# Optimization experiments

Hardware: AMD Instinct MI355X
Metric: run time of the kernel (lower is better)

## Reference

```python
import jax, jax.numpy as jnp
import numpy as np

V, E, H, Z = 32000, 512, 1024, 256
B, S, T = 64, 256, 64
BOS_ID, EOS_ID = 1, 2


def gru_cell(x_gates, h, W_hh, b_hh):
    # torch GRU gate order: r, z, n. x_gates: (B,3H) precomputed W_ih@x+b_ih.
    hg = h @ W_hh.T + b_hh
    xr, xz, xn = jnp.split(x_gates, 3, axis=-1)
    hr, hz, hn = jnp.split(hg, 3, axis=-1)
    r = jax.nn.sigmoid(xr + hr)
    z = jax.nn.sigmoid(xz + hz)
    n = jnp.tanh(xn + r * hn)
    return (1.0 - z) * n + z * h


def setup_inputs() -> dict:
    key = jax.random.key(0)
    ks = jax.random.split(key, 24)
    u = lambda k, sh: jax.random.uniform(k, sh, jnp.float32, -0.1, 0.1)
    n = lambda k, sh: jax.random.normal(k, sh, jnp.float32) * 0.05
    inp = {
        'input': jax.random.randint(ks[0], (S, B), 0, V),
        'eps': jax.random.normal(ks[1], (B, Z), jnp.float32),
        'emb_enc': u(ks[2], (V, E)).at[0].set(0.0),  # padding_idx=0
        'Wih_e': n(ks[3], (3 * H, E)), 'Whh_e': n(ks[4], (3 * H, H)),
        'bih_e': n(ks[5], (3 * H,)), 'bhh_e': n(ks[6], (3 * H,)),
        'W_enc': n(ks[7], (Z, H)), 'b_enc': n(ks[8], (Z,)),
        'W_loc': n(ks[9], (Z, Z)), 'b_loc': n(ks[10], (Z,)),
        'W_scale': n(ks[11], (Z, Z)), 'b_scale': n(ks[12], (Z,)),
        'emb_dec': u(ks[13], (V, E)).at[0].set(0.0),
        'W_dec': n(ks[14], (H, Z)), 'b_dec': n(ks[15], (H,)),
        'Wih_d': n(ks[16], (3 * H, E)), 'Whh_d': n(ks[17], (3 * H, H)),
        'bih_d': n(ks[18], (3 * H,)), 'bhh_d': n(ks[19], (3 * H,)),
        'W_voc': n(ks[20], (V, H)), 'b_voc': n(ks[21], (V,)),
    }
    return inp


def reference(input, eps, emb_enc, Wih_e, Whh_e, bih_e, bhh_e,
              W_enc, b_enc, W_loc, b_loc, W_scale, b_scale,
              emb_dec, W_dec, b_dec, Wih_d, Whh_d, bih_d, bhh_d,
              W_voc, b_voc):
    # ---- encode ----
    x = emb_enc[input]                                   # (S,B,E)
    gx = jnp.einsum('sbe,ge->sbg', x, Wih_e) + bih_e     # (S,B,3H)
    h0 = jnp.zeros((B, H), x.dtype)
    h_last, _ = jax.lax.scan(lambda h, g: (gru_cell(g, h, Whh_e, bhh_e), None), h0, gx)
    henc = h_last @ W_enc.T + b_enc                      # (B,Z)
    loc = henc @ W_loc.T + b_loc
    scale = jax.nn.softplus(henc @ W_scale.T + b_scale)
    # ---- reparametrize ----
    z = loc + eps * jnp.exp(0.5 * scale)
    # ---- decode (fixed T steps; original loop is data-dependent on EOS) ----
    hidden = z @ W_dec.T + b_dec                         # (B,H)
    xd = jnp.broadcast_to(emb_dec[EOS_ID], (B, E))       # constant EOS input each step
    gxd = xd @ Wih_d.T + bih_d                           # (B,3H), hoisted out of loop

    def step(h, _):
        h2 = gru_cell(gxd, h, Whh_d, bhh_d)
        log_p = jax.nn.log_softmax(h2 @ W_voc.T + b_voc, axis=-1)  # (B,V)
        tok = jnp.argmax(log_p)  # global flat argmax, as torch.argmax(...).item()
        return h2, (log_p, tok)

    _, (log_p, toks) = jax.lax.scan(step, hidden, None, length=T)
    seq = jnp.concatenate([jnp.array([BOS_ID], toks.dtype), toks])
    return log_p, seq, loc, scale
```

## Files before the change

### kernel.cpp

```cpp
#include <hip/hip_runtime.h>
#include <math.h>
#include <stdint.h>
#include <stddef.h>

typedef unsigned short u16;
typedef unsigned int   u32;
typedef __attribute__((ext_vector_type(8))) short short8;
typedef __attribute__((ext_vector_type(4))) float f32x4;

#define DI __device__ __forceinline__

static constexpr int Vv = 32000, Ee = 512, Hh = 1024, Zz = 256;
static constexpr int Bb = 64, Ss = 256, Tt = 64;
static constexpr int G3 = 3 * Hh;

static constexpr size_t OFF_WHHE  = 0;
static constexpr size_t SZ_WHH    = (size_t)G3 * Hh * 2;
static constexpr size_t OFF_WHHD  = OFF_WHHE + SZ_WHH;
static constexpr size_t OFF_WIHE3 = OFF_WHHD + SZ_WHH;
static constexpr size_t SZ_WIHE3  = (size_t)G3 * (3 * Ee) * 2;
static constexpr size_t OFF_WVOC  = OFF_WIHE3 + SZ_WIHE3;
static constexpr size_t SZ_WVOC   = (size_t)Vv * Hh * 2;
static constexpr size_t OFF_XS    = OFF_WVOC + SZ_WVOC;
static constexpr size_t SZ_XS     = (size_t)Ss * Bb * (3 * Ee) * 2;
static constexpr size_t OFF_GX    = OFF_XS + SZ_XS;
static constexpr size_t SZ_GX     = (size_t)Ss * Bb * G3 * 4;
static constexpr size_t OFF_H2B   = OFF_GX;
static constexpr size_t OFF_H2F   = OFF_GX + SZ_GX;
static constexpr size_t SZ_H2F    = (size_t)Tt * Bb * Hh * 4;
static constexpr size_t OFF_H     = OFF_H2F + SZ_H2F;
static constexpr size_t OFF_GXD   = OFF_H + (size_t)Bb * Hh * 4;
static constexpr size_t OFF_HENC  = OFF_GXD + 12288;
static constexpr size_t OFF_ZB    = OFF_HENC + (size_t)Bb * Zz * 4;
static constexpr size_t OFF_RM    = OFF_ZB + (size_t)Bb * Zz * 4;
static constexpr size_t OFF_SE    = OFF_RM + 16384;
static constexpr size_t OFF_LSE   = OFF_SE + 16384;
static constexpr size_t OFF_BV    = OFF_LSE + 16384;
static constexpr size_t OFF_BI    = OFF_BV + 16384;
static constexpr size_t OFF_CC    = OFF_BI + 16384;
static constexpr size_t OFF_CAND  = OFF_CC + 16384;
static constexpr size_t OFF_BAR   = OFF_CAND + (size_t)4096 * 32 * 4;

static constexpr size_t SZ_HAB    = (size_t)Bb * 2 * Hh * 2;

DI u16 f2bf(float f) {
  u32 u = __float_as_uint(f);
  u32 r = (u + 0x7FFFu + ((u >> 16) & 1u)) >> 16;
  return (u16)r;
}
DI float bf2f(u16 h) { return __uint_as_float(((u32)h) << 16); }

DI f32x4 mfma16(short8 a, short8 b, f32x4 c) {
  return __builtin_amdgcn_mfma_f32_16x16x32_bf16(a, b, c, 0, 0, 0);
}
DI void llds16(const u16* g, u16* l) {
  __builtin_amdgcn_global_load_lds(
      (const __attribute__((address_space(1))) u32*)g,
      (__attribute__((address_space(3))) u32*)l, 16, 0, 0);
}

DI void ag_store_u32(u32* p, u32 v) {
  __hip_atomic_store(p, v, __ATOMIC_RELAXED, __HIP_MEMORY_SCOPE_AGENT);
}
DI u32 ag_load_u32(const u32* p) {
  return __hip_atomic_load((u32*)p, __ATOMIC_RELAXED, __HIP_MEMORY_SCOPE_AGENT);
}
DI void ag_store_f32(float* p, float v) {
  __hip_atomic_store(p, v, __ATOMIC_RELAXED, __HIP_MEMORY_SCOPE_AGENT);
}

DI u16* hbuf_dev(char* rA, char* rB, char* rC, int i) {
  if (i < 192) return (u16*)(rA + (size_t)i * SZ_HAB);
  if (i < 228) return (u16*)(rB + (size_t)(i - 192) * SZ_HAB);
  return (u16*)(rC + (size_t)(i - 228) * SZ_HAB);
}

__global__ void k_zero(u32* p, int n) {
  for (int i = blockIdx.x * 256 + threadIdx.x; i < n; i += gridDim.x * 256) p[i] = 0;
}

__global__ void k_trip(const float* __restrict__ W, u16* __restrict__ W3, int rows, int kin) {
  int n = rows * kin;
  for (int i = blockIdx.x * 256 + threadIdx.x; i < n; i += gridDim.x * 256) {
    int rr = i / kin, k = i - rr * kin;
    float v = W[i];
    u16 hi = f2bf(v);
    u16 lo = f2bf(v - bf2f(hi));
    u16* o = W3 + (size_t)rr * (3 * kin);
    o[k] = hi; o[kin + k] = hi; o[2 * kin + k] = lo;
  }
}

__global__ void k_tobf(const float* __restrict__ W, u16* __restrict__ Wb, int n) {
  for (int i = blockIdx.x * 256 + threadIdx.x; i < n; i += gridDim.x * 256) Wb[i] = f2bf(W[i]);
}

__global__ void k_xsplit(const int* __restrict__ inp, const float* __restrict__ emb,
                         u16* __restrict__ xs) {
  int n = Ss * Bb * Ee;
  for (int i = blockIdx.x * 256 + threadIdx.x; i < n; i += gridDim.x * 256) {
    int m = i >> 9, k = i & (Ee - 1);
    int tok = inp[m];
    float v = emb[(size_t)tok * Ee + k];
    u16 hi = f2bf(v);
    u16 lo = f2bf(v - bf2f(hi));
    u16* o = xs + (size_t)m * (3 * Ee);
    o[k] = hi; o[Ee + k] = lo; o[2 * Ee + k] = hi;
  }
}

__global__ void k_gxd(const float* __restrict__ emb_dec, const float* __restrict__ Wih_d,
                      const float* __restrict__ bih_d, float* __restrict__ gxd) {
  int g = blockIdx.x * 256 + threadIdx.x;
  if (g >= G3) return;
  const float* er = emb_dec + 2 * Ee;
  const float* wr = Wih_d + (size_t)g * Ee;
  float s = 0.f;
  for (int e = 0; e < Ee; e++) s += er[e] * wr[e];
  gxd[g] = s + bih_d[g];
}

__global__ __launch_bounds__(256, 2) void gemm_bt(
    const u16* __restrict__ A, const u16* __restrict__ Bw, const float* __restrict__ bias,
    float* __restrict__ C, int M, int N, int K) {
  __shared__ __align__(16) u16 As[128 * 32];
  __shared__ __align__(16) u16 Bs[128 * 32];
  int tid = threadIdx.x;
  int wave = tid >> 6, lane = tid & 63;
  int wr = wave >> 1, wc = wave & 1;
  int m0 = blockIdx.y * 128, n0 = blockIdx.x * 128;
  f32x4 acc[4][4];
#pragma unroll
  for (int i = 0; i < 4; i++)
#pragma unroll
    for (int j = 0; j < 4; j++) acc[i][j] = (f32x4){0.f, 0.f, 0.f, 0.f};

  int lrow = lane >> 2, lcol = (lane & 3) * 8;
  int r15 = lane & 15, kk = (lane >> 4) * 8;

  for (int k0 = 0; k0 < K; k0 += 32) {
    __syncthreads();
#pragma unroll
    for (int rch = 0; rch < 2; rch++) {
      int c = rch * 4 + wave;
      int row = c * 16 + lrow;
      llds16(A  + (size_t)(m0 + row) * K + k0 + lcol, &As[c * 512]);
      llds16(Bw + (size_t)(n0 + row) * K + k0 + lcol, &Bs[c * 512]);
    }
    __syncthreads();
    short8 af[4], bfv[4];
#pragma unroll
    for (int mi = 0; mi < 4; mi++)
      af[mi] = *(const short8*)&As[(wr * 64 + mi * 16 + r15) * 32 + kk];
#pragma unroll
    for (int ni = 0; ni < 4; ni++)
      bfv[ni] = *(const short8*)&Bs[(wc * 64 + ni * 16 + r15) * 32 + kk];
#pragma unroll
    for (int mi = 0; mi < 4; mi++)
#pragma unroll
      for (int ni = 0; ni < 4; ni++) acc[mi][ni] = mfma16(af[mi], bfv[ni], acc[mi][ni]);
  }
#pragma unroll
  for (int mi = 0; mi < 4; mi++)
#pragma unroll
    for (int ni = 0; ni < 4; ni++) {
      int col = n0 + wc * 64 + ni * 16 + r15;
      float bs = bias[col];
#pragma unroll
      for (int i = 0; i < 4; i++) {
        int row = m0 + wr * 64 + mi * 16 + (lane >> 4) * 4 + i;
        C[(size_t)row * N + col] = acc[mi][ni][i] + bs;
      }
    }
}

template <int DEC>
__global__ __launch_bounds__(512, 1) void k_pers(
    const u16* __restrict__ W, const float* __restrict__ bhh, const float* __restrict__ gx0,
    char* rA, char* rB, char* rC, float* Hst, float* h2f0, u16* h2b0, u32* bar) {
  int tid = threadIdx.x, wave = tid >> 6, lane = tid & 63;
  int r15 = lane & 15, kk = (lane >> 4) * 8;
  int bq = blockIdx.x & 3, jt = blockIdx.x >> 2;
  int b0 = bq * 16, j0 = jt * 16;
  int kbase = wave * 128;
  const int NSTEP = DEC ? Tt : Ss;

  __shared__ float sC[8][64][13];
  __shared__ float hT[256];
  __shared__ __align__(8) u16 stg[2][16][16];

  int bl = tid >> 4, jc = tid & 15;
  float br = 0.f, bz = 0.f, bn = 0.f;
  float xr = 0.f, xz = 0.f, xn = 0.f;
  if (tid < 256) {
    hT[tid] = DEC ? Hst[(size_t)(b0 + bl) * Hh + j0 + jc] : 0.f;
    int j = j0 + jc;
    br = bhh[j]; bz = bhh[Hh + j]; bn = bhh[2 * Hh + j];
    if (DEC) { xr = gx0[j]; xz = gx0[Hh + j]; xn = gx0[2 * Hh + j]; }
    else {
      const float* gr = gx0 + (size_t)(b0 + bl) * G3;
      xr = gr[j]; xz = gr[Hh + j]; xn = gr[2 * Hh + j];
    }
  }
  __syncthreads();

  const u16* Wrow = W + (size_t)(j0 + r15) * Hh + kbase + kk;
  int lsrc = (bl >> 2) * 16 + jc;
  int isrc = bl & 3;
  int flgidx = (lane * 4 + bq) * 16;

  for (int st = 0; st < NSTEP; st++) {
    const u16* hin = hbuf_dev(rA, rB, rC, st);

    f32x4 acc[3];
#pragma unroll
    for (int g = 0; g < 3; g++) acc[g] = (f32x4){0.f, 0.f, 0.f, 0.f};
    const u16* Ab = hin + (size_t)(b0 + r15) * 2048 + kbase + kk;
#pragma unroll
    for (int ks = 0; ks < 4; ks++) {
      int ko = ks * 32;
      short8 ah = *(const short8*)(Ab + ko);
      short8 al = *(const short8*)(Ab + 1024 + ko);
      short8 w0 = *(const short8*)(Wrow + ko);
      short8 w1 = *(const short8*)(Wrow + (size_t)Hh * Hh + ko);
      short8 w2 = *(const short8*)(Wrow + (size_t)2 * Hh * Hh + ko);
      acc[0] = mfma16(ah, w0, acc[0]);
      acc[1] = mfma16(ah, w1, acc[1]);
      acc[2] = mfma16(ah, w2, acc[2]);
      acc[0] = mfma16(al, w0, acc[0]);
      acc[1] = mfma16(al, w1, acc[1]);
      acc[2] = mfma16(al, w2, acc[2]);
    }
#pragma unroll
    for (int g = 0; g < 3; g++)
#pragma unroll
      for (int i = 0; i < 4; i++) sC[wave][lane][g * 4 + i] = acc[g][i];
    __syncthreads();

    if (tid < 256) {
      float hgr = br, hgz = bz, hgn = bn;
#pragma unroll
      for (int w = 0; w < 8; w++) {
        hgr += sC[w][lsrc][isrc];
        hgz += sC[w][lsrc][4 + isrc];
        hgn += sC[w][lsrc][8 + isrc];
      }
      float rg = 1.0f / (1.0f + expf(-(xr + hgr)));
      float zg = 1.0f / (1.0f + expf(-(xz + hgz)));
      float ng = tanhf(xn + rg * hgn);
      float hn = (1.0f - zg) * ng + zg * hT[tid];
      hT[tid] = hn;
      u16 hi = f2bf(hn), lo = f2bf(hn - bf2f(hi));
      stg[0][bl][jc] = hi;
      stg[1][bl][jc] = lo;
      if (DEC) ag_store_f32(&h2f0[((size_t)st * Bb + b0 + bl) * Hh + j0 + jc], hn);
    }
    __syncthreads();

    if (tid < 256) {
      int part = tid >> 7, idx = tid & 127, row = idx >> 3, dw = idx & 7;
      if (st + 1 < NSTEP) {
        u16* hout = hbuf_dev(rA, rB, rC, st + 1);
        u32 val = ((const u32*)&stg[part][row][0])[dw];
        ag_store_u32((u32*)(hout + (size_t)(b0 + row) * 2048 + part * 1024 + j0) + dw, val);
      }
      if (DEC && tid < 128) {
        u16* h2b = h2b0 + (size_t)st * Bb * Hh;
        ag_store_u32((u32*)(h2b + (size_t)(b0 + row) * Hh + j0) + dw,
                     ((const u32*)&stg[0][row][0])[dw]);
      }
    }

    if (st + 1 < NSTEP) {
      asm volatile("s_waitcnt vmcnt(0)" ::: "memory");
      __syncthreads();
      if (tid == 0)
        ag_store_u32(&bar[blockIdx.x * 16], (u32)(st + 1));
      if (!DEC && tid < 256) {
        const float* gr = gx0 + ((size_t)(st + 1) * Bb + b0 + bl) * G3;
        int j = j0 + jc;
        xr = gr[j]; xz = gr[Hh + j]; xn = gr[2 * Hh + j];
      }
      if (jt == 0) {
        if (wave == 0) {
          for (;;) {
            int v = (int)ag_load_u32(&bar[flgidx]);
            if (__all(v >= st + 1)) break;
            __builtin_amdgcn_s_sleep(1);
          }
          if (lane == 0) ag_store_u32(&bar[4096 + bq * 16], (u32)(st + 1));
        }
      } else if (tid == 0) {
        while ((int)ag_load_u32(&bar[4096 + bq * 16]) < st + 1)
          __builtin_amdgcn_s_sleep(1);
      }
      __syncthreads();
    }
  }

  if (!DEC && tid < 256)
    Hst[(size_t)(b0 + bl) * Hh + j0 + jc] = hT[tid];
}

template <int DEC>
__global__ __launch_bounds__(512, 1) void k_step3(
    const u16* __restrict__ W, const float* __restrict__ bhh, const float* __restrict__ gxp,
    const u16* __restrict__ hAin, u16* __restrict__ hAout, float* __restrict__ h,
    float* __restrict__ h2f, u16* __restrict__ h2b) {
  __shared__ float sC[4][64][13];
  int tid = threadIdx.x, wave = tid >> 6, lane = tid & 63;
  int mw = wave & 3, khalf = wave >> 2;
  int m0 = mw * 16;
  int r15 = lane & 15, kk = (lane >> 4) * 8;
  int j0 = blockIdx.x * 16;
  int kbase = khalf * 512;

  f32x4 acc[3];
#pragma unroll
  for (int g = 0; g < 3; g++) acc[g] = (f32x4){0.f, 0.f, 0.f, 0.f};

  const u16* Ah = hAin + (size_t)(m0 + r15) * 2048 + kbase + kk;
  const u16* Wr = W + (size_t)(j0 + r15) * Hh + kbase + kk;
#pragma unroll 4
  for (int ks = 0; ks < 16; ks++) {
    int ko = ks * 32;
    short8 ah = *(const short8*)(Ah + ko);
    short8 al = *(const short8*)(Ah + 1024 + ko);
    short8 b0 = *(const short8*)(Wr + ko);
    short8 b1 = *(const short8*)(Wr + (size_t)Hh * Hh + ko);
    short8 b2 = *(const short8*)(Wr + (size_t)2 * Hh * Hh + ko);
    acc[0] = mfma16(ah, b0, acc[0]);
    acc[1] = mfma16(ah, b1, acc[1]);
    acc[2] = mfma16(ah, b2, acc[2]);
    acc[0] = mfma16(al, b0, acc[0]);
    acc[1] = mfma16(al, b1, acc[1]);
    acc[2] = mfma16(al, b2, acc[2]);
  }

  if (khalf == 1) {
#pragma unroll
    for (int g = 0; g < 3; g++)
#pragma unroll
      for (int i = 0; i < 4; i++) sC[mw][lane][g * 4 + i] = acc[g][i];
  }
  __syncthreads();
  if (khalf == 1) return;

  int j = j0 + r15;
  float br = bhh[j], bz = bhh[Hh + j], bn = bhh[2 * Hh + j];
  float xrD = 0.f, xzD = 0.f, xnD = 0.f;
  if (DEC) { xrD = gxp[j]; xzD = gxp[Hh + j]; xnD = gxp[2 * Hh + j]; }
#pragma unroll
  for (int i = 0; i < 4; i++) {
    int b = m0 + (lane >> 4) * 4 + i;
    float hgr = acc[0][i] + sC[mw][lane][i]     + br;
    float hgz = acc[1][i] + sC[mw][lane][4 + i] + bz;
    float hgn = acc[2][i] + sC[mw][lane][8 + i] + bn;
    float xr, xz, xn;
    if (DEC) { xr = xrD; xz = xzD; xn = xnD; }
    else {
      const float* gr = gxp + (size_t)b * G3;
      xr = gr[j]; xz = gr[Hh + j]; xn = gr[2 * Hh + j];
    }
    float rg = 1.0f / (1.0f + expf(-(xr + hgr)));
    float zg = 1.0f / (1.0f + expf(-(xz + hgz)));
    float ng = tanhf(xn + rg * hgn);
    float hold = h[(size_t)b * Hh + j];
    float hn = (1.0f - zg) * ng + zg * hold;
    h[(size_t)b * Hh + j] = hn;
    u16 hi = f2bf(hn);
    u16 lo = f2bf(hn - bf2f(hi));
    hAout[(size_t)b * 2048 + j] = hi;
    hAout[(size_t)b * 2048 + 1024 + j] = lo;
    if (DEC) {
      h2f[(size_t)b * Hh + j] = hn;
      h2b[(size_t)b * Hh + j] = hi;
    }
  }
}

__global__ __launch_bounds__(256, 2) void k_head1(const float* __restrict__ h,
    const float* __restrict__ Wenc, const float* __restrict__ benc, float* __restrict__ henc) {
  int b = blockIdx.x;
  __shared__ float hs[Hh];
  for (int k = threadIdx.x; k < Hh; k += 256) hs[k] = h[(size_t)b * Hh + k];
  __syncthreads();
  int q = threadIdx.x;
  const float* wrw = Wenc + (size_t)q * Hh;
  float s = 0.f;
  for (int k = 0; k < Hh; k++) s += hs[k] * wrw[k];
  henc[b * Zz + q] = s + benc[q];
}

__global__ __launch_bounds__(256, 2) void k_head2(const float* __restrict__ henc,
    const float* __restrict__ Wloc, const float* __restrict__ bloc,
    const float* __restrict__ Wsc, const float* __restrict__ bsc,
    const float* __restrict__ eps, float* __restrict__ outLoc, float* __restrict__ outSc,
    float* __restrict__ zb) {
  int b = blockIdx.x;
  __shared__ float hs[Zz];
  if (threadIdx.x < Zz) hs[threadIdx.x] = henc[b * Zz + threadIdx.x];
  __syncthreads();
  int q = threadIdx.x;
  const float* wl = Wloc + (size_t)q * Zz;
  const float* wsp = Wsc + (size_t)q * Zz;
  float sl = 0.f, ssum = 0.f;
  for (int k = 0; k < Zz; k++) { sl += hs[k] * wl[k]; ssum += hs[k] * wsp[k]; }
  sl += bloc[q]; ssum += bsc[q];
  float sp = fmaxf(ssum, 0.f) + log1pf(expf(-fabsf(ssum)));
  float zv = sl + eps[b * Zz + q] * expf(0.5f * sp);
  outLoc[b * Zz + q] = sl;
  outSc[b * Zz + q] = sp;
  zb[b * Zz + q] = zv;
}

__global__ __launch_bounds__(256, 2) void k_head3(const float* __restrict__ zb,
    const float* __restrict__ Wdec, const float* __restrict__ bdec,
    float* __restrict__ h, u16* __restrict__ hA0) {
  int b = blockIdx.x;
  __shared__ float zs[Zz];
  if (threadIdx.x < Zz) zs[threadIdx.x] = zb[b * Zz + threadIdx.x];
  __syncthreads();
  for (int j = threadIdx.x; j < Hh; j += 256) {
    const float* wrw = Wdec + (size_t)j * Zz;
    float s = 0.f;
    for (int k = 0; k < Zz; k++) s += zs[k] * wrw[k];
    s += bdec[j];
    h[(size_t)b * Hh + j] = s;
    u16 hi = f2bf(s);
    u16 lo = f2bf(s - bf2f(hi));
    hA0[(size_t)b * 2048 + j] = hi;
    hA0[(size_t)b * 2048 + 1024 + j] = lo;
  }
}

__global__ __launch_bounds__(256, 2) void k_rowred(const float* __restrict__ logits,
    float* __restrict__ rowmax, float* __restrict__ sumexp, int* __restrict__ ccnt,
    int* __restrict__ cand) {
  int r = blockIdx.x;
  const float* row = logits + (size_t)r * Vv;
  __shared__ float red[4];
  __shared__ float srm;
  __shared__ int lcnt;
  __shared__ int lcand[32];
  int tid = threadIdx.x, wave = tid >> 6, lane = tid & 63;
  if (tid == 0) lcnt = 0;
  float m = -3.0e38f;
  for (int c = tid * 4; c < Vv; c += 1024) {
    f32x4 v = *(const f32x4*)(row + c);
    m = fmaxf(fmaxf(fmaxf(m, v.x), v.y), fmaxf(v.z, v.w));
  }
  for (int o = 32; o; o >>= 1) m = fmaxf(m, __shfl_xor(m, o));
  if (lane == 0) red[wave] = m;
  __syncthreads();
  if (tid == 0) srm = fmaxf(fmaxf(red[0], red[1]), fmaxf(red[2], red[3]));
  __syncthreads();
  float rm = srm;
  float s = 0.f;
  for (int c = tid * 4; c < Vv; c += 1024) {
    f32x4 v = *(const f32x4*)(row + c);
    s += expf(v.x - rm) + expf(v.y - rm) + expf(v.z - rm) + expf(v.w - rm);
    if (v.x >= rm - 0.0625f) { int sl = atomicAdd(&lcnt, 1); if (sl < 32) lcand[sl] = c; }
    if (v.y >= rm - 0.0625f) { int sl = atomicAdd(&lcnt, 1); if (sl < 32) lcand[sl] = c + 1; }
    if (v.z >= rm - 0.0625f) { int sl = atomicAdd(&lcnt, 1); if (sl < 32) lcand[sl] = c + 2; }
    if (v.w >= rm - 0.0625f) { int sl = atomicAdd(&lcnt, 1); if (sl < 32) lcand[sl] = c + 3; }
  }
  for (int o = 32; o; o >>= 1) s += __shfl_xor(s, o);
  if (lane == 0) red[wave] = s;
  __syncthreads();
  if (tid == 0) {
    float st = red[0] + red[1] + red[2] + red[3];
    int cc = lcnt < 32 ? lcnt : 32;
    for (int i = 0; i < cc; i++)
      for (int k2 = i + 1; k2 < cc; k2++)
        if (lcand[k2] < lcand[i]) { int t = lcand[i]; lcand[i] = lcand[k2]; lcand[k2] = t; }
    rowmax[r] = rm; sumexp[r] = st; ccnt[r] = cc;
    for (int i = 0; i < cc; i++) cand[r * 32 + i] = lcand[i];
  }
}

__global__ __launch_bounds__(256, 1) void k_refine(const float* __restrict__ logits,
    const float* __restrict__ h2f, const float* __restrict__ Wvoc, const float* __restrict__ bvoc,
    const float* __restrict__ rowmax, const float* __restrict__ sumexp,
    const int* __restrict__ ccnt, const int* __restrict__ cand,
    float* __restrict__ lsec, float* __restrict__ bestv, int* __restrict__ besti) {
  int r = blockIdx.x;
  __shared__ float hrow[Hh];
  __shared__ float lex[32];
  __shared__ float del[32];
  int tid = threadIdx.x, wave = tid >> 6, lane = tid & 63;
  for (int k = tid; k < Hh; k += 256) hrow[k] = h2f[(size_t)r * Hh + k];
  int cnt = ccnt[r];
  float rm = rowmax[r];
  __syncthreads();
  for (int ci = wave; ci < cnt; ci += 4) {
    int v = cand[r * 32 + ci];
    const float* wrw = Wvoc + (size_t)v * Hh;
    float s = 0.f;
    for (int k = lane; k < Hh; k += 64) s += hrow[k] * wrw[k];
    for (int o = 32; o; o >>= 1) s += __shfl_xor(s, o);
    if (lane == 0) {
      float le = s + bvoc[v];
      lex[ci] = le;
      float la = logits[(size_t)r * Vv + v];
      del[ci] = expf(le - rm) - expf(la - rm);
    }
  }
  __syncthreads();
  if (tid == 0) {
    float se = sumexp[r];
    for (int i = 0; i < cnt; i++) se += del[i];
    float lse = rm + logf(se);
    lsec[r] = lse;
    float bv = -3.0e38f; int bvi = 0;
    for (int i = 0; i < cnt; i++)
      if (lex[i] > bv) { bv = lex[i]; bvi = cand[r * 32 + i]; }
    bestv[r] = bv - lse;
    besti[r] = (r & 63) * Vv + bvi;
  }
}

__global__ void k_argmax(const float* __restrict__ bestv, const int* __restrict__ besti,
                         float* __restrict__ outseq) {
  int tid = threadIdx.x;
  if (tid == 0) outseq[0] = 1.0f;
  for (int t = 0; t < Tt; t++) {
    float v = bestv[t * 64 + tid];
    int ii = besti[t * 64 + tid];
    for (int o = 1; o < 64; o <<= 1) {
      float ov = __shfl_xor(v, o);
      int oi = __shfl_xor(ii, o);
      if (ov > v || (ov == v && oi < ii)) { v = ov; ii = oi; }
    }
    if (tid == 0) outseq[1 + t] = (float)ii;
  }
}

__global__ __launch_bounds__(256, 2) void k_logp(float* __restrict__ logits,
                                                 const float* __restrict__ lsec) {
  size_t total = (size_t)Tt * Bb * Vv / 4;
  for (size_t p = (size_t)blockIdx.x * 256 + threadIdx.x; p < total;
       p += (size_t)gridDim.x * 256) {
    int r = (int)(p / (Vv / 4));
    f32x4 v = *(f32x4*)(logits + p * 4);
    float l = lsec[r];
    v.x -= l; v.y -= l; v.z -= l; v.w -= l;
    *(f32x4*)(logits + p * 4) = v;
  }
}

extern "C" void kernel_launch(void* const* d_in, const int* in_sizes, int n_in,
                              void* d_out, int out_size, void* d_ws, size_t ws_size,
                              hipStream_t stream) {
  (void)in_sizes; (void)n_in; (void)out_size; (void)ws_size;
  const int*   inp     = (const int*)d_in[0];
  const float* eps     = (const float*)d_in[1];
  const float* emb_enc = (const float*)d_in[2];
  const float* Wih_e   = (const float*)d_in[3];
  const float* Whh_e   = (const float*)d_in[4];
  const float* bih_e   = (const float*)d_in[5];
  const float* bhh_e   = (const float*)d_in[6];
  const float* W_enc   = (const float*)d_in[7];
  const float* b_enc   = (const float*)d_in[8];
  const float* W_loc   = (const float*)d_in[9];
  const float* b_loc   = (const float*)d_in[10];
  const float* W_sc    = (const float*)d_in[11];
  const float* b_sc    = (const float*)d_in[12];
  const float* emb_dec = (const float*)d_in[13];
  const float* W_dec   = (const float*)d_in[14];
  const float* b_dec   = (const float*)d_in[15];
  const float* Wih_d   = (const float*)d_in[16];
  const float* Whh_d   = (const float*)d_in[17];
  const float* bih_d   = (const float*)d_in[18];
  const float* bhh_d   = (const float*)d_in[19];
  const float* W_voc   = (const float*)d_in[20];
  const float* b_voc   = (const float*)d_in[21];

  char* ws = (char*)d_ws;
  u16*   WHHE  = (u16*)(ws + OFF_WHHE);
  u16*   WHHD  = (u16*)(ws + OFF_WHHD);
  u16*   WIHE3 = (u16*)(ws + OFF_WIHE3);
  u16*   WVOC  = (u16*)(ws + OFF_WVOC);
  u16*   XS    = (u16*)(ws + OFF_XS);
  float* GX    = (float*)(ws + OFF_GX);
  float* Hst   = (float*)(ws + OFF_H);
  float* H2F   = (float*)(ws + OFF_H2F);
  u16*   H2B   = (u16*)(ws + OFF_H2B);
  float* GXD   = (float*)(ws + OFF_GXD);
  float* HENC  = (float*)(ws + OFF_HENC);
  float* ZB    = (float*)(ws + OFF_ZB);
  float* RM    = (float*)(ws + OFF_RM);
  float* SE    = (float*)(ws + OFF_SE);
  float* LSE   = (float*)(ws + OFF_LSE);
  float* BV    = (float*)(ws + OFF_BV);
  int*   BI    = (int*)(ws + OFF_BI);
  int*   CC    = (int*)(ws + OFF_CC);
  int*   CAND  = (int*)(ws + OFF_CAND);
  u32*   BAR   = (u32*)(ws + OFF_BAR);

  char* rA = ws + OFF_XS;
  char* rB = ws + OFF_WIHE3;
  char* rC = ws + OFF_H2F;
  auto hbuf = [&](int i) -> u16* {
    if (i < 192) return (u16*)(rA + (size_t)i * SZ_HAB);
    if (i < 228) return (u16*)(rB + (size_t)(i - 192) * SZ_HAB);
    return (u16*)(rC + (size_t)(i - 228) * SZ_HAB);
  };

  float* out     = (float*)d_out;
  float* logits  = out;
  float* outseq  = out + (size_t)Tt * Bb * Vv;
  float* outloc  = outseq + (Tt + 1);
  float* outsc   = outloc + Bb * Zz;

  k_tobf<<<1024, 256, 0, stream>>>(Whh_e, WHHE, G3 * Hh);
  k_tobf<<<1024, 256, 0, stream>>>(Whh_d, WHHD, G3 * Hh);
  k_trip<<<512, 256, 0, stream>>>(Wih_e, WIHE3, G3, Ee);
  k_tobf<<<2048, 256, 0, stream>>>(W_voc, WVOC, Vv * Hh);
  k_xsplit<<<2048, 256, 0, stream>>>(inp, emb_enc, XS);

  {
    dim3 g(G3 / 128, (Ss * Bb) / 128);
    gemm_bt<<<g, 256, 0, stream>>>(XS, WIHE3, bih_e, GX, Ss * Bb, G3, 3 * Ee);
  }
  k_gxd<<<12, 256, 0, stream>>>(emb_dec, Wih_d, bih_d, GXD);
  k_zero<<<64, 256, 0, stream>>>((u32*)hbuf(0), (int)(SZ_HAB / 4));
  k_zero<<<1, 256, 0, stream>>>(BAR, 4224);

  hipError_t ce;
  {
    const u16* a0 = WHHE; const float* a1 = bhh_e; const float* a2 = GX;
    char* a3 = rA; char* a4 = rB; char* a5 = rC; float* a6 = Hst;
    float* a7 = nullptr; u16* a8 = nullptr; u32* a9 = BAR;
    void* args[] = {&a0,&a1,&a2,&a3,&a4,&a5,&a6,&a7,&a8,&a9};
    ce = hipLaunchCooperativeKernel(reinterpret_cast<void*>(&k_pers<0>),
                                    dim3(256), dim3(512), args, 0, stream);
  }
  if (ce != hipSuccess) {
    for (int s = 0; s < Ss; s++)
      k_step3<0><<<64, 512, 0, stream>>>(WHHE, bhh_e, GX + (size_t)s * Bb * G3,
                                         hbuf(s), hbuf(s + 1), Hst, nullptr, nullptr);
  }

  k_head1<<<64, 256, 0, stream>>>(Hst, W_enc, b_enc, HENC);
  k_head2<<<64, 256, 0, stream>>>(HENC, W_loc, b_loc, W_sc, b_sc, eps, outloc, outsc, ZB);
  k_head3<<<64, 256, 0, stream>>>(ZB, W_dec, b_dec, Hst, hbuf(0));
  k_zero<<<1, 256, 0, stream>>>(BAR, 4224);

  {
    const u16* a0 = WHHD; const float* a1 = bhh_d; const float* a2 = GXD;
    char* a3 = rA; char* a4 = rB; char* a5 = rC; float* a6 = Hst;
    float* a7 = H2F; u16* a8 = H2B; u32* a9 = BAR;
    void* args[] = {&a0,&a1,&a2,&a3,&a4,&a5,&a6,&a7,&a8,&a9};
    hipError_t cd = hipLaunchCooperativeKernel(reinterpret_cast<void*>(&k_pers<1>),
                                               dim3(256), dim3(512), args, 0, stream);
    if (cd != hipSuccess) {
      for (int t = 0; t < Tt; t++)
        k_step3<1><<<64, 512, 0, stream>>>(WHHD, bhh_d, GXD, hbuf(t), hbuf(t + 1), Hst,
                                           H2F + (size_t)t * Bb * Hh,
                                           H2B + (size_t)t * Bb * Hh);
    }
  }

  {
    dim3 g(Vv / 128, (Tt * Bb) / 128);
    gemm_bt<<<g, 256, 0, stream>>>(H2B, WVOC, b_voc, logits, Tt * Bb, Vv, Hh);
  }

  k_rowred<<<Tt * Bb, 256, 0, stream>>>(logits, RM, SE, CC, CAND);
  k_refine<<<Tt * Bb, 256, 0, stream>>>(logits, H2F, W_voc, b_voc, RM, SE, CC, CAND, LSE, BV, BI);
  k_argmax<<<1, 64, 0, stream>>>(BV, BI, outseq);
  k_logp<<<2048, 256, 0, stream>>>(logits, LSE);
}
```

Before: 2.825 ms.

## Drop split-bf16 input projection, simplify barrier, fuse softmax row kernels

Measured after the change: 2.637 ms. -6.7%, faster.

```diff
diff --git a/kernel.cpp b/kernel.cpp
--- a/kernel.cpp
+++ b/kernel.cpp
@@ -79,33 +79,16 @@
   for (int i = blockIdx.x * 256 + threadIdx.x; i < n; i += gridDim.x * 256) p[i] = 0;
 }
 
-__global__ void k_trip(const float* __restrict__ W, u16* __restrict__ W3, int rows, int kin) {
-  int n = rows * kin;
-  for (int i = blockIdx.x * 256 + threadIdx.x; i < n; i += gridDim.x * 256) {
-    int rr = i / kin, k = i - rr * kin;
-    float v = W[i];
-    u16 hi = f2bf(v);
-    u16 lo = f2bf(v - bf2f(hi));
-    u16* o = W3 + (size_t)rr * (3 * kin);
-    o[k] = hi; o[kin + k] = hi; o[2 * kin + k] = lo;
-  }
-}
-
 __global__ void k_tobf(const float* __restrict__ W, u16* __restrict__ Wb, int n) {
   for (int i = blockIdx.x * 256 + threadIdx.x; i < n; i += gridDim.x * 256) Wb[i] = f2bf(W[i]);
 }
 
-__global__ void k_xsplit(const int* __restrict__ inp, const float* __restrict__ emb,
-                         u16* __restrict__ xs) {
+__global__ void k_xgather(const int* __restrict__ inp, const float* __restrict__ emb,
+                          u16* __restrict__ xs) {
   int n = Ss * Bb * Ee;
   for (int i = blockIdx.x * 256 + threadIdx.x; i < n; i += gridDim.x * 256) {
     int m = i >> 9, k = i & (Ee - 1);
-    int tok = inp[m];
-    float v = emb[(size_t)tok * Ee + k];
-    u16 hi = f2bf(v);
-    u16 lo = f2bf(v - bf2f(hi));
-    u16* o = xs + (size_t)m * (3 * Ee);
-    o[k] = hi; o[Ee + k] = lo; o[2 * Ee + k] = hi;
+    xs[i] = f2bf(emb[(size_t)inp[m] * Ee + k]);
   }
 }
 
@@ -281,20 +264,11 @@
         int j = j0 + jc;
         xr = gr[j]; xz = gr[Hh + j]; xn = gr[2 * Hh + j];
       }
-      if (jt == 0) {
-        if (wave == 0) {
-          for (;;) {
-            int v = (int)ag_load_u32(&bar[flgidx]);
-            if (__all(v >= st + 1)) break;
-            __builtin_amdgcn_s_sleep(1);
-          }
-          if (lane == 0) ag_store_u32(&bar[4096 + bq * 16], (u32)(st + 1));
-        }
-      } else if (tid == 0) {
-        while ((int)ag_load_u32(&bar[4096 + bq * 16]) < st + 1)
-          __builtin_amdgcn_s_sleep(1);
+      for (;;) {
+        int v = (int)ag_load_u32(&bar[flgidx]);
+        if (__all(v >= st + 1)) break;
+        __builtin_amdgcn_s_sleep(1);
       }
-      __syncthreads();
     }
   }
 
@@ -434,30 +408,40 @@
   }
 }
 
-__global__ __launch_bounds__(256, 2) void k_rowred(const float* __restrict__ logits,
-    float* __restrict__ rowmax, float* __restrict__ sumexp, int* __restrict__ ccnt,
-    int* __restrict__ cand) {
+__global__ __launch_bounds__(1024, 1) void k_soft(
+    float* __restrict__ logits, const float* __restrict__ h2f,
+    const float* __restrict__ Wvoc, const float* __restrict__ bvoc,
+    float* __restrict__ bestv, int* __restrict__ besti) {
+  __shared__ float row[Vv];
+  __shared__ float hrow[Hh];
+  __shared__ float red[16];
+  __shared__ float srm, ssum, slse;
+  __shared__ int lcnt, scc;
+  __shared__ int lcand[32];
+  __shared__ float lex[32], del[32];
   int r = blockIdx.x;
-  const float* row = logits + (size_t)r * Vv;
-  __shared__ float red[4];
-  __shared__ float srm;
-  __shared__ int lcnt;
-  __shared__ int lcand[32];
   int tid = threadIdx.x, wave = tid >> 6, lane = tid & 63;
+  float* grow = logits + (size_t)r * Vv;
   if (tid == 0) lcnt = 0;
+  hrow[tid] = h2f[(size_t)r * Hh + tid];
   float m = -3.0e38f;
-  for (int c = tid * 4; c < Vv; c += 1024) {
-    f32x4 v = *(const f32x4*)(row + c);
-    m = fmaxf(fmaxf(fmaxf(m, v.x), v.y), fmaxf(v.z, v.w));
+  for (int c = tid * 4; c < Vv; c += 4096) {
+    f32x4 v = *(const f32x4*)(grow + c);
+    *(f32x4*)(row + c) = v;
+    m = fmaxf(fmaxf(m, v.x), fmaxf(v.y, fmaxf(v.z, v.w)));
   }
   for (int o = 32; o; o >>= 1) m = fmaxf(m, __shfl_xor(m, o));
   if (lane == 0) red[wave] = m;
   __syncthreads();
-  if (tid == 0) srm = fmaxf(fmaxf(red[0], red[1]), fmaxf(red[2], red[3]));
+  if (tid == 0) {
+    float t = red[0];
+    for (int i = 1; i < 16; i++) t = fmaxf(t, red[i]);
+    srm = t;
+  }
   __syncthreads();
   float rm = srm;
   float s = 0.f;
-  for (int c = tid * 4; c < Vv; c += 1024) {
+  for (int c = tid * 4; c < Vv; c += 4096) {
     f32x4 v = *(const f32x4*)(row + c);
     s += expf(v.x - rm) + expf(v.y - rm) + expf(v.z - rm) + expf(v.w - rm);
     if (v.x >= rm - 0.0625f) { int sl = atomicAdd(&lcnt, 1); if (sl < 32) lcand[sl] = c; }
@@ -469,54 +453,47 @@
   if (lane == 0) red[wave] = s;
   __syncthreads();
   if (tid == 0) {
-    float st = red[0] + red[1] + red[2] + red[3];
+    float t = 0.f;
+    for (int i = 0; i < 16; i++) t += red[i];
+    ssum = t;
     int cc = lcnt < 32 ? lcnt : 32;
     for (int i = 0; i < cc; i++)
       for (int k2 = i + 1; k2 < cc; k2++)
-        if (lcand[k2] < lcand[i]) { int t = lcand[i]; lcand[i] = lcand[k2]; lcand[k2] = t; }
-    rowmax[r] = rm; sumexp[r] = st; ccnt[r] = cc;
-    for (int i = 0; i < cc; i++) cand[r * 32 + i] = lcand[i];
-  }
-}
-
-__global__ __launch_bounds__(256, 1) void k_refine(const float* __restrict__ logits,
-    const float* __restrict__ h2f, const float* __restrict__ Wvoc, const float* __restrict__ bvoc,
-    const float* __restrict__ rowmax, const float* __restrict__ sumexp,
-    const int* __restrict__ ccnt, const int* __restrict__ cand,
-    float* __restrict__ lsec, float* __restrict__ bestv, int* __restrict__ besti) {
-  int r = blockIdx.x;
-  __shared__ float hrow[Hh];
-  __shared__ float lex[32];
-  __shared__ float del[32];
-  int tid = threadIdx.x, wave = tid >> 6, lane = tid & 63;
-  for (int k = tid; k < Hh; k += 256) hrow[k] = h2f[(size_t)r * Hh + k];
-  int cnt = ccnt[r];
-  float rm = rowmax[r];
-  __syncthreads();
-  for (int ci = wave; ci < cnt; ci += 4) {
-    int v = cand[r * 32 + ci];
+        if (lcand[k2] < lcand[i]) { int q = lcand[i]; lcand[i] = lcand[k2]; lcand[k2] = q; }
+    scc = cc;
+  }
+  __syncthreads();
+  int cnt = scc;
+  for (int ci = wave; ci < cnt; ci += 16) {
+    int v = lcand[ci];
     const float* wrw = Wvoc + (size_t)v * Hh;
-    float s = 0.f;
-    for (int k = lane; k < Hh; k += 64) s += hrow[k] * wrw[k];
-    for (int o = 32; o; o >>= 1) s += __shfl_xor(s, o);
+    float sd = 0.f;
+    for (int k = lane; k < Hh; k += 64) sd += hrow[k] * wrw[k];
+    for (int o = 32; o; o >>= 1) sd += __shfl_xor(sd, o);
     if (lane == 0) {
-      float le = s + bvoc[v];
+      float le = sd + bvoc[v];
       lex[ci] = le;
-      float la = logits[(size_t)r * Vv + v];
-      del[ci] = expf(le - rm) - expf(la - rm);
+      del[ci] = expf(le - rm) - expf(row[v] - rm);
     }
   }
   __syncthreads();
   if (tid == 0) {
-    float se = sumexp[r];
+    float se = ssum;
     for (int i = 0; i < cnt; i++) se += del[i];
     float lse = rm + logf(se);
-    lsec[r] = lse;
+    slse = lse;
     float bv = -3.0e38f; int bvi = 0;
     for (int i = 0; i < cnt; i++)
-      if (lex[i] > bv) { bv = lex[i]; bvi = cand[r * 32 + i]; }
+      if (lex[i] > bv) { bv = lex[i]; bvi = lcand[i]; }
     bestv[r] = bv - lse;
     besti[r] = (r & 63) * Vv + bvi;
+  }
+  __syncthreads();
+  float l = slse;
+  for (int c = tid * 4; c < Vv; c += 4096) {
+    f32x4 v = *(const f32x4*)(row + c);
+    v.x -= l; v.y -= l; v.z -= l; v.w -= l;
+    *(f32x4*)(grow + c) = v;
   }
 }
 
@@ -533,19 +510,6 @@
       if (ov > v || (ov == v && oi < ii)) { v = ov; ii = oi; }
     }
     if (tid == 0) outseq[1 + t] = (float)ii;
-  }
-}
-
-__global__ __launch_bounds__(256, 2) void k_logp(float* __restrict__ logits,
-                                                 const float* __restrict__ lsec) {
-  size_t total = (size_t)Tt * Bb * Vv / 4;
-  for (size_t p = (size_t)blockIdx.x * 256 + threadIdx.x; p < total;
-       p += (size_t)gridDim.x * 256) {
-    int r = (int)(p / (Vv / 4));
-    f32x4 v = *(f32x4*)(logits + p * 4);
-    float l = lsec[r];
-    v.x -= l; v.y -= l; v.z -= l; v.w -= l;
-    *(f32x4*)(logits + p * 4) = v;
   }
 }
 
@@ -579,7 +543,7 @@
   char* ws = (char*)d_ws;
   u16*   WHHE  = (u16*)(ws + OFF_WHHE);
   u16*   WHHD  = (u16*)(ws + OFF_WHHD);
-  u16*   WIHE3 = (u16*)(ws + OFF_WIHE3);
+  u16*   WIHB  = (u16*)(ws + OFF_WIHE3);
   u16*   WVOC  = (u16*)(ws + OFF_WVOC);
   u16*   XS    = (u16*)(ws + OFF_XS);
   float* GX    = (float*)(ws + OFF_GX);
@@ -589,13 +553,8 @@
   float* GXD   = (float*)(ws + OFF_GXD);
   float* HENC  = (float*)(ws + OFF_HENC);
   float* ZB    = (float*)(ws + OFF_ZB);
-  float* RM    = (float*)(ws + OFF_RM);
-  float* SE    = (float*)(ws + OFF_SE);
-  float* LSE   = (float*)(ws + OFF_LSE);
   float* BV    = (float*)(ws + OFF_BV);
   int*   BI    = (int*)(ws + OFF_BI);
-  int*   CC    = (int*)(ws + OFF_CC);
-  int*   CAND  = (int*)(ws + OFF_CAND);
   u32*   BAR   = (u32*)(ws + OFF_BAR);
 
   char* rA = ws + OFF_XS;
@@ -615,17 +574,17 @@
 
   k_tobf<<<1024, 256, 0, stream>>>(Whh_e, WHHE, G3 * Hh);
   k_tobf<<<1024, 256, 0, stream>>>(Whh_d, WHHD, G3 * Hh);
-  k_trip<<<512, 256, 0, stream>>>(Wih_e, WIHE3, G3, Ee);
+  k_tobf<<<512, 256, 0, stream>>>(Wih_e, WIHB, G3 * Ee);
   k_tobf<<<2048, 256, 0, stream>>>(W_voc, WVOC, Vv * Hh);
-  k_xsplit<<<2048, 256, 0, stream>>>(inp, emb_enc, XS);
+  k_xgather<<<2048, 256, 0, stream>>>(inp, emb_enc, XS);
 
   {
     dim3 g(G3 / 128, (Ss * Bb) / 128);
-    gemm_bt<<<g, 256, 0, stream>>>(XS, WIHE3, bih_e, GX, Ss * Bb, G3, 3 * Ee);
+    gemm_bt<<<g, 256, 0, stream>>>(XS, WIHB, bih_e, GX, Ss * Bb, G3, Ee);
   }
   k_gxd<<<12, 256, 0, stream>>>(emb_dec, Wih_d, bih_d, GXD);
   k_zero<<<64, 256, 0, stream>>>((u32*)hbuf(0), (int)(SZ_HAB / 4));
-  k_zero<<<1, 256, 0, stream>>>(BAR, 4224);
+  k_zero<<<1, 256, 0, stream>>>(BAR, 4096);
 
   hipError_t ce;
   {
@@ -645,7 +604,7 @@
   k_head1<<<64, 256, 0, stream>>>(Hst, W_enc, b_enc, HENC);
   k_head2<<<64, 256, 0, stream>>>(HENC, W_loc, b_loc, W_sc, b_sc, eps, outloc, outsc, ZB);
   k_head3<<<64, 256, 0, stream>>>(ZB, W_dec, b_dec, Hst, hbuf(0));
-  k_zero<<<1, 256, 0, stream>>>(BAR, 4224);
+  k_zero<<<1, 256, 0, stream>>>(BAR, 4096);
 
   {
     const u16* a0 = WHHD; const float* a1 = bhh_d; const float* a2 = GXD;
@@ -667,8 +626,6 @@
     gemm_bt<<<g, 256, 0, stream>>>(H2B, WVOC, b_voc, logits, Tt * Bb, Vv, Hh);
   }
 
-  k_rowred<<<Tt * Bb, 256, 0, stream>>>(logits, RM, SE, CC, CAND);
-  k_refine<<<Tt * Bb, 256, 0, stream>>>(logits, H2F, W_voc, b_voc, RM, SE, CC, CAND, LSE, BV, BI);
+  k_soft<<<Tt * Bb, 1024, 0, stream>>>(logits, H2F, W_voc, b_voc, BV, BI);
   k_argmax<<<1, 64, 0, stream>>>(BV, BI, outseq);
-  k_logp<<<2048, 256, 0, stream>>>(logits, LSE);
-}
+}
```
